# Kernel optimization log

Hardware: AMD Instinct MI355X
Metric: run time of the kernel (lower is better)

Reference implementation:

```python
import jax, jax.numpy as jnp
import numpy as np

B, T, D, S = 4, 8192, 512, 16

def setup_inputs() -> dict:
    key = jax.random.key(0)
    k1, k2, k3, k4, k5 = jax.random.split(key, 5)
    x = jax.random.normal(k1, (B, T, D), dtype=jnp.float32)
    # splat parameters as in __init__: centers ~ 0.02*randn, log_scales = 0
    centers = jax.random.normal(k2, (S, D), dtype=jnp.float32) * 0.02
    log_scales = jnp.zeros((S,), dtype=jnp.float32)
    # xavier-uniform linear weights (gain = 1/(1+layer_idx*0.1) = 1.0 for layer 0)
    limit = float(np.sqrt(6.0 / (D + D)))
    Wv = jax.random.uniform(k3, (D, D), minval=-limit, maxval=limit, dtype=jnp.float32)
    Wo = jax.random.uniform(k4, (D, D), minval=-limit, maxval=limit, dtype=jnp.float32)
    return {"x": x, "centers": centers, "log_scales": log_scales, "Wv": Wv, "Wo": Wo}

def reference(x, centers, log_scales, Wv, Wo):
    # scales clamped as in EnhancedAdaptiveSplat.get_scale
    scales = jnp.clip(jnp.exp(log_scales), 0.1, 2.0)           # [S]
    v = jnp.einsum('btd,ed->bte', x, Wv)                       # value projection [B,T,D]
    # squared distance token<->splat via expansion (no [B,T,S,D] intermediate)
    x2 = jnp.sum(x * x, axis=-1, keepdims=True)                # [B,T,1]
    c2 = jnp.sum(centers * centers, axis=-1)                   # [S]
    xc = jnp.einsum('btd,sd->bts', x, centers)                 # [B,T,S]
    d2 = x2 + c2 - 2.0 * xc                                    # [B,T,S]
    logits = -0.5 * d2 / (scales * scales)                     # gaussian kernel log-weights
    attn = jax.nn.softmax(logits, axis=-1)                     # normalize over splats [B,T,S]
    # tokens -> splats aggregation, then splats -> tokens distribution
    splat_states = jnp.einsum('bts,btd->bsd', attn, v)         # [B,S,D]
    out = jnp.einsum('bts,bsd->btd', attn, splat_states)       # [B,T,D]
    return jnp.einsum('btd,ed->bte', out, Wo)                  # output projection
```

## Files before the change

kernel.cpp:

```cpp
#include <hip/hip_runtime.h>
#include <hip/hip_bf16.h>
#include <math.h>

#define B_ 4
#define T_ 8192
#define D_ 512
#define S_ 16

__device__ __forceinline__ float reduce_scatter16(float vals[S_], int lane) {
  {
    const int bit = (lane >> 5) & 1;
#pragma unroll
    for (int i = 0; i < 8; ++i) {
      float send = bit ? vals[i] : vals[i + 8];
      float keep = bit ? vals[i + 8] : vals[i];
      vals[i] = keep + __shfl_xor(send, 32, 64);
    }
  }
  {
    const int bit = (lane >> 4) & 1;
#pragma unroll
    for (int i = 0; i < 4; ++i) {
      float send = bit ? vals[i] : vals[i + 4];
      float keep = bit ? vals[i + 4] : vals[i];
      vals[i] = keep + __shfl_xor(send, 16, 64);
    }
  }
  {
    const int bit = (lane >> 3) & 1;
#pragma unroll
    for (int i = 0; i < 2; ++i) {
      float send = bit ? vals[i] : vals[i + 2];
      float keep = bit ? vals[i + 2] : vals[i];
      vals[i] = keep + __shfl_xor(send, 8, 64);
    }
  }
  {
    const int bit = (lane >> 2) & 1;
    float send = bit ? vals[0] : vals[1];
    float keep = bit ? vals[1] : vals[0];
    float v = keep + __shfl_xor(send, 4, 64);
    v += __shfl_xor(v, 2, 64);
    v += __shfl_xor(v, 1, 64);
    return v;
  }
}

__device__ __forceinline__ float dot4(float4 a, float4 b) {
  return a.x * b.x + a.y * b.y + a.z * b.z + a.w * b.w;
}

__global__ __launch_bounds__(256, 2) void attn_ts_k(const float* __restrict__ x,
                                                    const float* __restrict__ centers,
                                                    const float* __restrict__ log_scales,
                                                    float* __restrict__ attn,
                                                    float* __restrict__ ts) {
  __shared__ __align__(16) float a_s[64][S_];
  const int lane = threadIdx.x & 63;
  const int w = threadIdx.x >> 6;
  const int myS = (lane >> 2) & 15;
  const int b = blockIdx.x >> 7;
  const int t0 = (blockIdx.x & 127) * 64;

  {
    float4 c_reg[S_][2];
#pragma unroll
    for (int s = 0; s < S_; ++s)
#pragma unroll
      for (int j = 0; j < 2; ++j)
        c_reg[s][j] = *(const float4*)(centers + s * D_ + (j << 8) + (lane << 2));

    float c2;
    {
      float vals[S_];
#pragma unroll
      for (int s = 0; s < S_; ++s)
        vals[s] = dot4(c_reg[s][0], c_reg[s][0]) + dot4(c_reg[s][1], c_reg[s][1]);
      c2 = reduce_scatter16(vals, lane);
    }
    const float sc = fminf(fmaxf(__expf(log_scales[myS]), 0.1f), 2.0f);
    const float inv2 = 0.5f / (sc * sc);

    const int tw = t0 + (w << 4);
    const float* xr = x + ((size_t)b * T_ + tw) * D_;
    float* ar = attn + ((size_t)b * T_ + tw) * S_;

    float4 na0 = *(const float4*)(xr + (lane << 2));
    float4 na1 = *(const float4*)(xr + 256 + (lane << 2));
    float4 nb0 = *(const float4*)(xr + 512 + (lane << 2));
    float4 nb1 = *(const float4*)(xr + 768 + (lane << 2));

#pragma unroll 1
    for (int tt = 0; tt < 16; tt += 2) {
      float4 a0 = na0, a1 = na1, b0 = nb0, b1 = nb1;
      if (tt + 2 < 16) {
        const float* nx = xr + (size_t)(tt + 2) * D_;
        na0 = *(const float4*)(nx + (lane << 2));
        na1 = *(const float4*)(nx + 256 + (lane << 2));
        nb0 = *(const float4*)(nx + 512 + (lane << 2));
        nb1 = *(const float4*)(nx + 768 + (lane << 2));
      }

      float x2a = dot4(a0, a0) + dot4(a1, a1);
      float x2b = dot4(b0, b0) + dot4(b1, b1);

      float va[S_], vb[S_];
#pragma unroll
      for (int s = 0; s < S_; ++s) {
        va[s] = x2a - 2.f * (dot4(a0, c_reg[s][0]) + dot4(a1, c_reg[s][1]));
        vb[s] = x2b - 2.f * (dot4(b0, c_reg[s][0]) + dot4(b1, c_reg[s][1]));
      }

      float ra = reduce_scatter16(va, lane);
      float rb = reduce_scatter16(vb, lane);
      float la = -(ra + c2) * inv2;
      float lb = -(rb + c2) * inv2;

      float ma = la, mb = lb;
      ma = fmaxf(ma, __shfl_xor(ma, 4, 64));  mb = fmaxf(mb, __shfl_xor(mb, 4, 64));
      ma = fmaxf(ma, __shfl_xor(ma, 8, 64));  mb = fmaxf(mb, __shfl_xor(mb, 8, 64));
      ma = fmaxf(ma, __shfl_xor(ma, 16, 64)); mb = fmaxf(mb, __shfl_xor(mb, 16, 64));
      ma = fmaxf(ma, __shfl_xor(ma, 32, 64)); mb = fmaxf(mb, __shfl_xor(mb, 32, 64));
      float ea = __expf(la - ma), eb = __expf(lb - mb);
      float sa = ea, sb = eb;
      sa += __shfl_xor(sa, 4, 64);  sb += __shfl_xor(sb, 4, 64);
      sa += __shfl_xor(sa, 8, 64);  sb += __shfl_xor(sb, 8, 64);
      sa += __shfl_xor(sa, 16, 64); sb += __shfl_xor(sb, 16, 64);
      sa += __shfl_xor(sa, 32, 64); sb += __shfl_xor(sb, 32, 64);
      float aa = ea / sa, ab2 = eb / sb;

      if ((lane & 3) == 0) {
        ar[(size_t)tt * S_ + myS] = aa;
        ar[(size_t)(tt + 1) * S_ + myS] = ab2;
        a_s[(w << 4) + tt][myS] = aa;
        a_s[(w << 4) + tt + 1][myS] = ab2;
      }
    }
  }

  __syncthreads();

  {
    const int d = threadIdx.x;
    float2 acc[S_];
#pragma unroll
    for (int s = 0; s < S_; ++s) acc[s] = make_float2(0.f, 0.f);

    const float* xb = x + ((size_t)b * T_ + t0) * D_;

#pragma unroll 8
    for (int t = 0; t < 64; ++t) {
      float xv0 = xb[(size_t)t * D_ + d];
      float xv1 = xb[(size_t)t * D_ + d + 256];
      const float4* ap = (const float4*)a_s[t];
      float4 q0 = ap[0], q1 = ap[1], q2 = ap[2], q3 = ap[3];
      float av[S_] = {q0.x, q0.y, q0.z, q0.w, q1.x, q1.y, q1.z, q1.w,
                      q2.x, q2.y, q2.z, q2.w, q3.x, q3.y, q3.z, q3.w};
#pragma unroll
      for (int s = 0; s < S_; ++s) {
        acc[s].x += av[s] * xv0;
        acc[s].y += av[s] * xv1;
      }
    }

    float* tb = ts + (size_t)b * S_ * D_;
#pragma unroll
    for (int s = 0; s < S_; ++s) {
      atomicAdd(tb + s * D_ + d, acc[s].x);
      atomicAdd(tb + s * D_ + d + 256, acc[s].y);
    }
  }
}

__global__ __launch_bounds__(256) void proj_k(const float* __restrict__ in,
                                              const float* __restrict__ W,
                                              float* __restrict__ out) {
  __shared__ float red[4][64];
  const int r = blockIdx.x >> 3;
  const int eb = blockIdx.x & 7;
  const int el = threadIdx.x & 63;
  const int kc = threadIdx.x >> 6;
  const int e = (eb << 6) + el;

  const float4* w4 = (const float4*)(W + (size_t)e * D_ + kc * 128);
  const float4* i4 = (const float4*)(in + (size_t)r * D_ + kc * 128);
  float acc = 0.f;
#pragma unroll
  for (int k = 0; k < 32; ++k) acc += dot4(w4[k], i4[k]);

  red[kc][el] = acc;
  __syncthreads();
  if (kc == 0)
    out[(size_t)r * D_ + e] = red[0][el] + red[1][el] + red[2][el] + red[3][el];
}

#define K4_TOK 64
__global__ __launch_bounds__(256) void out_k(const float* __restrict__ attn,
                                             const float* __restrict__ ss_o,
                                             float* __restrict__ out) {
  const int chunks = T_ / K4_TOK;
  const int b = blockIdx.x / chunks;
  const int t0 = (blockIdx.x % chunks) * K4_TOK;
  const int w = threadIdx.x >> 6;
  const int lane = threadIdx.x & 63;
  const int e0 = (w << 7) + (lane << 1);

  float2 ssf[S_];
  const float* sb = ss_o + (size_t)b * S_ * D_;
#pragma unroll
  for (int s = 0; s < S_; ++s) ssf[s] = *(const float2*)(sb + s * D_ + e0);

  const float4* ab = (const float4*)(attn + ((size_t)b * T_ + t0) * S_);
  float* ob = out + ((size_t)b * T_ + t0) * D_ + e0;

#pragma unroll 4
  for (int t = 0; t < K4_TOK; ++t) {
    float4 a0 = ab[t * 4 + 0], a1 = ab[t * 4 + 1];
    float4 a2 = ab[t * 4 + 2], a3 = ab[t * 4 + 3];
    float av[S_] = {a0.x, a0.y, a0.z, a0.w, a1.x, a1.y, a1.z, a1.w,
                    a2.x, a2.y, a2.z, a2.w, a3.x, a3.y, a3.z, a3.w};
    float2 acc = make_float2(0.f, 0.f);
#pragma unroll
    for (int s = 0; s < S_; ++s) {
      acc.x += av[s] * ssf[s].x;
      acc.y += av[s] * ssf[s].y;
    }
    *(float2*)(ob + (size_t)t * D_) = acc;
  }
}

extern "C" void kernel_launch(void* const* d_in, const int* in_sizes, int n_in,
                              void* d_out, int out_size, void* d_ws, size_t ws_size,
                              hipStream_t stream) {
  const float* x          = (const float*)d_in[0];
  const float* centers    = (const float*)d_in[1];
  const float* log_scales = (const float*)d_in[2];
  const float* Wv         = (const float*)d_in[3];
  const float* Wo         = (const float*)d_in[4];
  float* out = (float*)d_out;

  float* attn = (float*)d_ws;
  float* ts   = attn + (size_t)B_ * T_ * S_;
  float* tmp  = ts + (size_t)B_ * S_ * D_;
  float* ss_o = tmp + (size_t)B_ * S_ * D_;

  hipMemsetAsync(ts, 0, (size_t)B_ * S_ * D_ * sizeof(float), stream);

  attn_ts_k<<<512, 256, 0, stream>>>(x, centers, log_scales, attn, ts);
  proj_k<<<512, 256, 0, stream>>>(ts, Wv, tmp);
  proj_k<<<512, 256, 0, stream>>>(tmp, Wo, ss_o);
  out_k<<<B_ * (T_ / K4_TOK), 256, 0, stream>>>(attn, ss_o, out);
}
```

Measured before the change: 177.5 us.

## Assign one lane per token-splat pair with centers in LDS and smaller chunks

The attention-weight phase is restructured so that each lane computes the full 512-long dot product for one (token, splat) pair. Centers are staged in padded shared memory instead of being held in registers, and the 16-way butterfly reduce-scatter is replaced with a short 16-lane softmax shuffle. The token chunk per block shrinks from 64 to 32, doubling the grid and raising the occupancy hint to 4 blocks per CU. In exchange, each x row is read by 16 lanes through uncoalesced strided float4 loads, and the number of atomicAdds into the splat accumulator doubles.

```diff
diff --git a/kernel.cpp b/kernel.cpp
--- a/kernel.cpp
+++ b/kernel.cpp
@@ -1,5 +1,4 @@
 #include <hip/hip_runtime.h>
-#include <hip/hip_bf16.h>
 #include <math.h>
 
 #define B_ 4
@@ -7,149 +6,101 @@
 #define D_ 512
 #define S_ 16
 
-__device__ __forceinline__ float reduce_scatter16(float vals[S_], int lane) {
-  {
-    const int bit = (lane >> 5) & 1;
-#pragma unroll
-    for (int i = 0; i < 8; ++i) {
-      float send = bit ? vals[i] : vals[i + 8];
-      float keep = bit ? vals[i + 8] : vals[i];
-      vals[i] = keep + __shfl_xor(send, 32, 64);
-    }
-  }
-  {
-    const int bit = (lane >> 4) & 1;
-#pragma unroll
-    for (int i = 0; i < 4; ++i) {
-      float send = bit ? vals[i] : vals[i + 4];
-      float keep = bit ? vals[i + 4] : vals[i];
-      vals[i] = keep + __shfl_xor(send, 16, 64);
-    }
-  }
-  {
-    const int bit = (lane >> 3) & 1;
-#pragma unroll
-    for (int i = 0; i < 2; ++i) {
-      float send = bit ? vals[i] : vals[i + 2];
-      float keep = bit ? vals[i + 2] : vals[i];
-      vals[i] = keep + __shfl_xor(send, 8, 64);
-    }
-  }
-  {
-    const int bit = (lane >> 2) & 1;
-    float send = bit ? vals[0] : vals[1];
-    float keep = bit ? vals[1] : vals[0];
-    float v = keep + __shfl_xor(send, 4, 64);
-    v += __shfl_xor(v, 2, 64);
-    v += __shfl_xor(v, 1, 64);
-    return v;
-  }
-}
+#define CHUNK 32
+
+#define CPAD 516
+
 
 __device__ __forceinline__ float dot4(float4 a, float4 b) {
   return a.x * b.x + a.y * b.y + a.z * b.z + a.w * b.w;
 }
 
-__global__ __launch_bounds__(256, 2) void attn_ts_k(const float* __restrict__ x,
+__global__ __launch_bounds__(256, 4) void attn_ts_k(const float* __restrict__ x,
                                                     const float* __restrict__ centers,
                                                     const float* __restrict__ log_scales,
                                                     float* __restrict__ attn,
                                                     float* __restrict__ ts) {
-  __shared__ __align__(16) float a_s[64][S_];
-  const int lane = threadIdx.x & 63;
-  const int w = threadIdx.x >> 6;
-  const int myS = (lane >> 2) & 15;
-  const int b = blockIdx.x >> 7;
-  const int t0 = (blockIdx.x & 127) * 64;
+  __shared__ __align__(16) float c_s[S_ * CPAD];
+  __shared__ __align__(16) float a_s[CHUNK][S_];
+  const int tid = threadIdx.x;
+  const int lane = tid & 63;
+  const int w = tid >> 6;
+  const int s = lane & 15;
+  const int tl = lane >> 4;
+  const int b = blockIdx.x >> 8;
+  const int t0 = (blockIdx.x & 255) * CHUNK;
+
+#pragma unroll
+  for (int j = 0; j < 8; ++j) {
+    int idx = j * 256 + tid;
+    int row = idx >> 7;
+    int col = idx & 127;
+    float4 v = ((const float4*)centers)[idx];
+    *(float4*)(&c_s[row * CPAD + (col << 2)]) = v;
+  }
+  __syncthreads();
+
+  float c2 = 0.f;
+#pragma unroll 4
+  for (int d = 0; d < D_; d += 4) {
+    float4 cv = *(const float4*)(&c_s[s * CPAD + d]);
+    c2 += dot4(cv, cv);
+  }
+
+  const float sc = fminf(fmaxf(__expf(log_scales[s]), 0.1f), 2.0f);
+  const float inv2 = 0.5f / (sc * sc);
+
+#pragma unroll 1
+  for (int pass = 0; pass < 2; ++pass) {
+    const int wtok = (w << 3) + (pass << 2) + tl;
+    const float* xrow = x + ((size_t)b * T_ + t0 + wtok) * D_;
+
+    float xc = 0.f, x2 = 0.f;
+#pragma unroll 1
+    for (int d = 0; d < D_; d += 16) {
+      float4 xa = *(const float4*)(xrow + d);
+      float4 xb = *(const float4*)(xrow + d + 4);
+      float4 xv = *(const float4*)(xrow + d + 8);
+      float4 xd = *(const float4*)(xrow + d + 12);
+      float4 ca = *(const float4*)(&c_s[s * CPAD + d]);
+      float4 cb = *(const float4*)(&c_s[s * CPAD + d + 4]);
+      float4 cc = *(const float4*)(&c_s[s * CPAD + d + 8]);
+      float4 cd = *(const float4*)(&c_s[s * CPAD + d + 12]);
+      xc += dot4(xa, ca) + dot4(xb, cb) + dot4(xv, cc) + dot4(xd, cd);
+      x2 += dot4(xa, xa) + dot4(xb, xb) + dot4(xv, xv) + dot4(xd, xd);
+    }
+
+    float logit = -(x2 + c2 - 2.f * xc) * inv2;
+
+    float m = logit;
+    m = fmaxf(m, __shfl_xor(m, 1, 64));
+    m = fmaxf(m, __shfl_xor(m, 2, 64));
+    m = fmaxf(m, __shfl_xor(m, 4, 64));
+    m = fmaxf(m, __shfl_xor(m, 8, 64));
+    float e = __expf(logit - m);
+    float sum = e;
+    sum += __shfl_xor(sum, 1, 64);
+    sum += __shfl_xor(sum, 2, 64);
+    sum += __shfl_xor(sum, 4, 64);
+    sum += __shfl_xor(sum, 8, 64);
+    float a = e / sum;
+
+    attn[((size_t)b * T_ + t0 + wtok) * S_ + s] = a;
+    a_s[wtok][s] = a;
+  }
+
+  __syncthreads();
 
   {
-    float4 c_reg[S_][2];
-#pragma unroll
-    for (int s = 0; s < S_; ++s)
-#pragma unroll
-      for (int j = 0; j < 2; ++j)
-        c_reg[s][j] = *(const float4*)(centers + s * D_ + (j << 8) + (lane << 2));
-
-    float c2;
-    {
-      float vals[S_];
-#pragma unroll
-      for (int s = 0; s < S_; ++s)
-        vals[s] = dot4(c_reg[s][0], c_reg[s][0]) + dot4(c_reg[s][1], c_reg[s][1]);
-      c2 = reduce_scatter16(vals, lane);
-    }
-    const float sc = fminf(fmaxf(__expf(log_scales[myS]), 0.1f), 2.0f);
-    const float inv2 = 0.5f / (sc * sc);
-
-    const int tw = t0 + (w << 4);
-    const float* xr = x + ((size_t)b * T_ + tw) * D_;
-    float* ar = attn + ((size_t)b * T_ + tw) * S_;
-
-    float4 na0 = *(const float4*)(xr + (lane << 2));
-    float4 na1 = *(const float4*)(xr + 256 + (lane << 2));
-    float4 nb0 = *(const float4*)(xr + 512 + (lane << 2));
-    float4 nb1 = *(const float4*)(xr + 768 + (lane << 2));
-
-#pragma unroll 1
-    for (int tt = 0; tt < 16; tt += 2) {
-      float4 a0 = na0, a1 = na1, b0 = nb0, b1 = nb1;
-      if (tt + 2 < 16) {
-        const float* nx = xr + (size_t)(tt + 2) * D_;
-        na0 = *(const float4*)(nx + (lane << 2));
-        na1 = *(const float4*)(nx + 256 + (lane << 2));
-        nb0 = *(const float4*)(nx + 512 + (lane << 2));
-        nb1 = *(const float4*)(nx + 768 + (lane << 2));
-      }
-
-      float x2a = dot4(a0, a0) + dot4(a1, a1);
-      float x2b = dot4(b0, b0) + dot4(b1, b1);
-
-      float va[S_], vb[S_];
-#pragma unroll
-      for (int s = 0; s < S_; ++s) {
-        va[s] = x2a - 2.f * (dot4(a0, c_reg[s][0]) + dot4(a1, c_reg[s][1]));
-        vb[s] = x2b - 2.f * (dot4(b0, c_reg[s][0]) + dot4(b1, c_reg[s][1]));
-      }
-
-      float ra = reduce_scatter16(va, lane);
-      float rb = reduce_scatter16(vb, lane);
-      float la = -(ra + c2) * inv2;
-      float lb = -(rb + c2) * inv2;
-
-      float ma = la, mb = lb;
-      ma = fmaxf(ma, __shfl_xor(ma, 4, 64));  mb = fmaxf(mb, __shfl_xor(mb, 4, 64));
-      ma = fmaxf(ma, __shfl_xor(ma, 8, 64));  mb = fmaxf(mb, __shfl_xor(mb, 8, 64));
-      ma = fmaxf(ma, __shfl_xor(ma, 16, 64)); mb = fmaxf(mb, __shfl_xor(mb, 16, 64));
-      ma = fmaxf(ma, __shfl_xor(ma, 32, 64)); mb = fmaxf(mb, __shfl_xor(mb, 32, 64));
-      float ea = __expf(la - ma), eb = __expf(lb - mb);
-      float sa = ea, sb = eb;
-      sa += __shfl_xor(sa, 4, 64);  sb += __shfl_xor(sb, 4, 64);
-      sa += __shfl_xor(sa, 8, 64);  sb += __shfl_xor(sb, 8, 64);
-      sa += __shfl_xor(sa, 16, 64); sb += __shfl_xor(sb, 16, 64);
-      sa += __shfl_xor(sa, 32, 64); sb += __shfl_xor(sb, 32, 64);
-      float aa = ea / sa, ab2 = eb / sb;
-
-      if ((lane & 3) == 0) {
-        ar[(size_t)tt * S_ + myS] = aa;
-        ar[(size_t)(tt + 1) * S_ + myS] = ab2;
-        a_s[(w << 4) + tt][myS] = aa;
-        a_s[(w << 4) + tt + 1][myS] = ab2;
-      }
-    }
-  }
-
-  __syncthreads();
-
-  {
-    const int d = threadIdx.x;
+    const int d = tid;
     float2 acc[S_];
 #pragma unroll
-    for (int s = 0; s < S_; ++s) acc[s] = make_float2(0.f, 0.f);
+    for (int si = 0; si < S_; ++si) acc[si] = make_float2(0.f, 0.f);
 
     const float* xb = x + ((size_t)b * T_ + t0) * D_;
 
-#pragma unroll 8
-    for (int t = 0; t < 64; ++t) {
+#pragma unroll 4
+    for (int t = 0; t < CHUNK; ++t) {
       float xv0 = xb[(size_t)t * D_ + d];
       float xv1 = xb[(size_t)t * D_ + d + 256];
       const float4* ap = (const float4*)a_s[t];
@@ -157,17 +108,17 @@
       float av[S_] = {q0.x, q0.y, q0.z, q0.w, q1.x, q1.y, q1.z, q1.w,
                       q2.x, q2.y, q2.z, q2.w, q3.x, q3.y, q3.z, q3.w};
 #pragma unroll
-      for (int s = 0; s < S_; ++s) {
-        acc[s].x += av[s] * xv0;
-        acc[s].y += av[s] * xv1;
+      for (int si = 0; si < S_; ++si) {
+        acc[si].x += av[si] * xv0;
+        acc[si].y += av[si] * xv1;
       }
     }
 
     float* tb = ts + (size_t)b * S_ * D_;
 #pragma unroll
-    for (int s = 0; s < S_; ++s) {
-      atomicAdd(tb + s * D_ + d, acc[s].x);
-      atomicAdd(tb + s * D_ + d + 256, acc[s].y);
+    for (int si = 0; si < S_; ++si) {
+      atomicAdd(tb + si * D_ + d, acc[si].x);
+      atomicAdd(tb + si * D_ + d + 256, acc[si].y);
     }
   }
 }
@@ -246,7 +197,7 @@
 
   hipMemsetAsync(ts, 0, (size_t)B_ * S_ * D_ * sizeof(float), stream);
 
-  attn_ts_k<<<512, 256, 0, stream>>>(x, centers, log_scales, attn, ts);
+  attn_ts_k<<<B_ * (T_ / CHUNK), 256, 0, stream>>>(x, centers, log_scales, attn, ts);
   proj_k<<<512, 256, 0, stream>>>(ts, Wv, tmp);
   proj_k<<<512, 256, 0, stream>>>(tmp, Wo, ss_o);
   out_k<<<B_ * (T_ / K4_TOK), 256, 0, stream>>>(attn, ss_o, out);
```

Result: slower. 207.6 us (+17.0%).
